# Optimization experiments

Measured on AMD Instinct MI355X. Metric: run time of the kernel, lower is better.

The kernel has to match this reference:

```python
import jax, jax.numpy as jnp
import numpy as np

# rate-1/2, constraint_length-3 generator polynomials (Sionna polynomial_selector),
# bit format MSB-first: first char multiplies the current input bit.
GEN_POLY = ("101", "111")


def make_trellis(gen_poly):
    """Build next-state and output-bit lookup tables for a non-recursive conv code.

    State s encodes the shift register [u[t-1], ..., u[t-mu]] with u[t-1] as MSB.
    """
    G = np.array([[int(c) for c in p] for p in gen_poly], dtype=np.int32)  # [n_out, L]
    L = G.shape[1]
    mu = L - 1                      # memory
    ns = 2 ** mu                    # number of trellis states
    next_state = np.zeros((ns, 2), np.int32)
    out_table = np.zeros((ns, 2, G.shape[0]), np.int32)
    for s in range(ns):
        sbits = [(s >> (mu - 1 - i)) & 1 for i in range(mu)]
        for b in (0, 1):
            reg = np.array([b] + sbits, np.int32)       # [u[t], u[t-1], ..., u[t-mu]]
            out_table[s, b] = (G @ reg) % 2             # one bit per polynomial
            next_state[s, b] = (b << (mu - 1)) | (s >> 1)
    return jnp.asarray(next_state), jnp.asarray(out_table)


def setup_inputs() -> dict:
    key = jax.random.key(0)
    B, K = 8192, 2048
    inputs = jax.random.randint(key, (B, K), 0, 2).astype(jnp.float32)
    next_state, out_table = make_trellis(GEN_POLY)
    return {"inputs": inputs, "next_state": next_state, "out_table": out_table}


def _encode(msg_bits, next_state, out_table):
    """msg_bits: [B, k] int32 in {0,1} -> codeword bits [B, k * n_out] int32."""
    B = msg_bits.shape[0]
    st0 = jnp.zeros((B,), jnp.int32)

    def step(st, u):
        # st, u: [B]; table lookups replace tf.gather_nd on to_nodes / op_mat
        out_bits = out_table[st, u]          # [B, n_out]
        return next_state[st, u], out_bits

    _, outs = jax.lax.scan(step, st0, msg_bits.T)      # outs: [k, B, n_out]
    # time-major interleaving: per symbol, n_out bits in polynomial order
    return jnp.transpose(outs, (1, 0, 2)).reshape(B, -1)


def reference(inputs, next_state, out_table):
    msg = inputs.astype(jnp.int32)                     # tf.cast(inputs, tf.int32)
    cw = _encode(msg, next_state, out_table)           # [B, n]
    return cw.astype(jnp.float32)
```

## Files before the change

### kernel.cpp

```cpp
#include <hip/hip_runtime.h>
#include <hip/hip_bf16.h>


#define K_MASK 2047

__global__ __launch_bounds__(256) void conv_enc_kernel(
    const unsigned int* __restrict__ in, unsigned int* __restrict__ out) {
    long tid = (long)blockIdx.x * blockDim.x + threadIdx.x;
    long e0 = tid << 1;

    uint2 v = reinterpret_cast<const uint2*>(in)[tid];

    unsigned int p2 = __shfl_up(v.x, 1);
    unsigned int p1 = __shfl_up(v.y, 1);
    if ((threadIdx.x & 63) == 0) {
        if ((e0 & K_MASK) == 0) {
            p1 = 0u; p2 = 0u;
        } else {
            p1 = in[e0 - 1];
            p2 = in[e0 - 2];
        }
    }

    uint4 o;
    o.x = v.x ^ p2;
    o.y = o.x ^ p1;
    o.z = v.y ^ p1;
    o.w = o.z ^ v.x;

    reinterpret_cast<uint4*>(out)[tid] = o;
}

extern "C" void kernel_launch(void* const* d_in, const int* in_sizes, int n_in,
                              void* d_out, int out_size, void* d_ws, size_t ws_size,
                              hipStream_t stream) {
    const unsigned int* in = (const unsigned int*)d_in[0];
    unsigned int* out = (unsigned int*)d_out;

    long total_threads = (long)in_sizes[0] / 2;
    int block = 256;
    int grid = (int)((total_threads + block - 1) / block);

    conv_enc_kernel<<<grid, block, 0, stream>>>(in, out);
}
```

Before: 36.19 us.

## Use grid-stride loop and reload previous pair instead of wave shuffles

Replaces the one-thread-per-pair launch with a fixed 4096-block grid-stride loop. Each iteration reloads the neighbouring uint2 from global memory, which should normally hit in cache, instead of fetching it with cross-lane shuffles plus a special path for lane 0. The aim is to drop the shuffle and divergent-branch overhead and to cut block scheduling cost. In exchange it issues one extra global load per pair and leaves the loop to the compiler.

```diff
diff --git a/kernel.cpp b/kernel.cpp
--- a/kernel.cpp
+++ b/kernel.cpp
@@ -2,44 +2,38 @@
 #include <hip/hip_bf16.h>
 
 
-#define K_MASK 2047
+__global__ __launch_bounds__(256) void conv_enc_kernel(
+    const uint2* __restrict__ in2, uint4* __restrict__ out4, int nPairs) {
+    int stride = gridDim.x * blockDim.x;
+    int idx = blockIdx.x * blockDim.x + threadIdx.x;
 
-__global__ __launch_bounds__(256) void conv_enc_kernel(
-    const unsigned int* __restrict__ in, unsigned int* __restrict__ out) {
-    long tid = (long)blockIdx.x * blockDim.x + threadIdx.x;
-    long e0 = tid << 1;
+    #pragma unroll 2
+    for (; idx < nPairs; idx += stride) {
+        uint2 v = in2[idx];
+        bool rs = (idx & 1023) == 0;
+        uint2 w = in2[rs ? idx : idx - 1];
+        unsigned int p2 = rs ? 0u : w.x;
+        unsigned int p1 = rs ? 0u : w.y;
 
-    uint2 v = reinterpret_cast<const uint2*>(in)[tid];
+        uint4 o;
+        o.x = v.x ^ p2;
+        o.y = o.x ^ p1;
+        o.z = v.y ^ p1;
+        o.w = o.z ^ v.x;
 
-    unsigned int p2 = __shfl_up(v.x, 1);
-    unsigned int p1 = __shfl_up(v.y, 1);
-    if ((threadIdx.x & 63) == 0) {
-        if ((e0 & K_MASK) == 0) {
-            p1 = 0u; p2 = 0u;
-        } else {
-            p1 = in[e0 - 1];
-            p2 = in[e0 - 2];
-        }
+        out4[idx] = o;
     }
-
-    uint4 o;
-    o.x = v.x ^ p2;
-    o.y = o.x ^ p1;
-    o.z = v.y ^ p1;
-    o.w = o.z ^ v.x;
-
-    reinterpret_cast<uint4*>(out)[tid] = o;
 }
 
 extern "C" void kernel_launch(void* const* d_in, const int* in_sizes, int n_in,
                               void* d_out, int out_size, void* d_ws, size_t ws_size,
                               hipStream_t stream) {
-    const unsigned int* in = (const unsigned int*)d_in[0];
-    unsigned int* out = (unsigned int*)d_out;
+    const uint2* in2 = (const uint2*)d_in[0];
+    uint4* out4 = (uint4*)d_out;
 
-    long total_threads = (long)in_sizes[0] / 2;
+    int nPairs = in_sizes[0] / 2;
     int block = 256;
-    int grid = (int)((total_threads + block - 1) / block);
+    int grid = 4096;
 
-    conv_enc_kernel<<<grid, block, 0, stream>>>(in, out);
+    conv_enc_kernel<<<grid, block, 0, stream>>>(in2, out4, nPairs);
 }
```

Measured after the change: 36.53 us. About the same (+0.9%).
